# Optimization experiments

Hardware: AMD Instinct MI355X
Metric: run time of the kernel (lower is better)

Reference implementation:

```python
import jax, jax.numpy as jnp
import numpy as np
from jax import lax

D_MODEL = 1024
D_STATE = 128
D_CONV = 4
EXPAND = 2
HEADDIM = 64
D_INNER = EXPAND * D_MODEL          # 2048
NHEADS = D_INNER // HEADDIM          # 32
CONV_DIM = D_INNER + 2 * D_STATE     # 2304
D_IN_PROJ = 2 * D_INNER + 2 * D_STATE + NHEADS  # 4384
B_SZ, L_SEQ = 4, 2048
EPS = 1e-5


def setup_inputs() -> dict:
    key = jax.random.key(0)
    ks = jax.random.split(key, 10)
    x = jax.random.normal(ks[0], (B_SZ, L_SEQ, D_MODEL), dtype=jnp.float32)
    in_proj_w = jax.random.normal(ks[1], (D_IN_PROJ, D_MODEL), dtype=jnp.float32) * 0.02
    conv_w = jax.random.normal(ks[2], (CONV_DIM, D_CONV), dtype=jnp.float32) * 0.2
    conv_b = jax.random.normal(ks[3], (CONV_DIM,), dtype=jnp.float32) * 0.02
    dt_bias = jax.random.normal(ks[4], (NHEADS,), dtype=jnp.float32) * 0.5
    A_log = jnp.log(jax.random.uniform(ks[5], (NHEADS,), minval=1.0, maxval=16.0, dtype=jnp.float32))
    D = 1.0 + 0.1 * jax.random.normal(ks[6], (NHEADS,), dtype=jnp.float32)
    norm_w = jnp.ones((D_INNER,), dtype=jnp.float32)
    out_proj_w = jax.random.normal(ks[7], (D_MODEL, D_INNER), dtype=jnp.float32) * 0.02
    ln_w = jnp.ones((D_MODEL,), dtype=jnp.float32)
    ln_b = jnp.zeros((D_MODEL,), dtype=jnp.float32)
    return {"x": x, "in_proj_w": in_proj_w, "conv_w": conv_w, "conv_b": conv_b,
            "dt_bias": dt_bias, "A_log": A_log, "D": D, "norm_w": norm_w,
            "out_proj_w": out_proj_w, "ln_w": ln_w, "ln_b": ln_b}


def _mamba_block(x, in_proj_w, conv_w, conv_b, dt_bias, A_log, D, norm_w, out_proj_w, ln_w, ln_b):
    b, l, _ = x.shape
    # 1. input projection -> z, xBC, dt
    zxbcdt = jnp.einsum('bld,ed->ble', x, in_proj_w)  # (b,l,D_IN_PROJ)
    z = zxbcdt[..., :D_INNER]
    xBC = zxbcdt[..., D_INNER:D_INNER + CONV_DIM]
    dt = jax.nn.softplus(zxbcdt[..., D_INNER + CONV_DIM:] + dt_bias)  # (b,l,H)
    # 2. causal depthwise conv1d + silu
    xBC_t = xBC.transpose(0, 2, 1)  # (b,CONV_DIM,l)
    conv = lax.conv_general_dilated(xBC_t, conv_w[:, None, :], (1,), [(D_CONV - 1, 0)],
                                    feature_group_count=CONV_DIM,
                                    dimension_numbers=('NCW', 'OIW', 'NCW'))
    xBC = jax.nn.silu(conv + conv_b[:, None]).transpose(0, 2, 1)  # (b,l,CONV_DIM)
    x_ssm = xBC[..., :D_INNER].reshape(b, l, NHEADS, HEADDIM)     # (b,l,h,p)
    Bm = xBC[..., D_INNER:D_INNER + D_STATE]                      # (b,l,n) ngroups=1
    Cm = xBC[..., D_INNER + D_STATE:]                             # (b,l,n)
    # 3. selective scan
    A = -jnp.exp(A_log)               # (h,)
    dA = jnp.exp(dt * A)              # (b,l,h)
    def step(h, inp):
        dA_t, x_t, B_t, C_t, dt_t = inp  # (b,h),(b,h,p),(b,n),(b,n),(b,h)
        dBx = dt_t[:, :, None, None] * x_t[..., None] * B_t[:, None, None, :]
        h = h * dA_t[:, :, None, None] + dBx                       # (b,h,p,n)
        y = jnp.einsum('bhpn,bn->bhp', h, C_t)
        return h, y
    h0 = jnp.zeros((b, NHEADS, HEADDIM, D_STATE), dtype=x.dtype)
    inputs = (dA.transpose(1, 0, 2), x_ssm.transpose(1, 0, 2, 3),
              Bm.transpose(1, 0, 2), Cm.transpose(1, 0, 2), dt.transpose(1, 0, 2))
    _, ys = lax.scan(step, h0, inputs)                             # (l,b,h,p)
    y = ys.transpose(1, 0, 2, 3) + D[None, None, :, None] * x_ssm  # skip D term
    y = y.reshape(b, l, D_INNER)
    # 4. gated RMSNorm (norm_before_gate=False): gate first, then normalize
    y = y * jax.nn.silu(z)
    y = y * lax.rsqrt(jnp.mean(y * y, axis=-1, keepdims=True) + EPS) * norm_w
    # 5. output projection + residual
    y = jnp.einsum('bld,ed->ble', y, out_proj_w) + x
    # 6. LayerNorm (dropout is identity in eval)
    mu = jnp.mean(y, axis=-1, keepdims=True)
    var = jnp.mean((y - mu) ** 2, axis=-1, keepdims=True)
    return (y - mu) * lax.rsqrt(var + EPS) * ln_w + ln_b


def reference(x, in_proj_w, conv_w, conv_b, dt_bias, A_log, D, norm_w, out_proj_w, ln_w, ln_b):
    return _mamba_block(x, in_proj_w, conv_w, conv_b, dt_bias, A_log, D, norm_w, out_proj_w, ln_w, ln_b)
```

## Files before the change

kernel.cpp:

```cpp
#include <hip/hip_runtime.h>

typedef unsigned short u16;
typedef unsigned int   u32;

#define L_SEQ    2048
#define D_MODEL  1024
#define D_STATE  128
#define D_INNER  2048
#define NHEADS   32
#define HEADDIM  64
#define CONV_DIM 2304
#define D_IN_PROJ 4384
#define EPSF     1e-5f
#define QC       128
#define NCH      16

using frag  = __attribute__((ext_vector_type(8))) short;
using f32x4 = __attribute__((ext_vector_type(4))) float;
typedef __attribute__((ext_vector_type(8))) unsigned short u16x8;

__device__ __forceinline__ u16 f2bf(float f) {
  u32 u = __float_as_uint(f);
  return (u16)((u + 0x7fffu + ((u >> 16) & 1u)) >> 16);
}
__device__ __forceinline__ float bf2f(u16 u) {
  return __uint_as_float(((u32)u) << 16);
}
__device__ __forceinline__ void async16(const void* g, void* l) {
  __builtin_amdgcn_global_load_lds((const __attribute__((address_space(1))) u32*)g,
                                   (__attribute__((address_space(3))) u32*)l, 16, 0, 0);
}

__global__ __launch_bounds__(256) void k_cvt_all(const float* __restrict__ x,
                                                 u16* __restrict__ xb,
                                                 const float* __restrict__ w1,
                                                 u16* __restrict__ w1b,
                                                 const float* __restrict__ w2,
                                                 u16* __restrict__ w2b) {
  int bid = blockIdx.x;
  int t = threadIdx.x;
  const float* src;
  u16* dst;
  int i;
  if (bid < 8192)       { i = bid * 256 + t;          src = x;  dst = xb;  }
  else if (bid < 12576) { i = (bid - 8192) * 256 + t; src = w1; dst = w1b; }
  else if (bid < 14624) { i = (bid - 12576) * 256 + t; src = w2; dst = w2b; }
  else {
    i = (bid - 14624) * 256 + t;
    ((ushort4*)(w1b + (size_t)4384 * 1024))[i] = ushort4{0, 0, 0, 0};
    return;
  }
  float4 v = ((const float4*)src)[i];
  ushort4 o;
  o.x = f2bf(v.x); o.y = f2bf(v.y); o.z = f2bf(v.z); o.w = f2bf(v.w);
  ((ushort4*)dst)[i] = o;
}

template <int MODE>
__global__ __launch_bounds__(256) void k_gemm(const u16* __restrict__ A,
                                              const u16* __restrict__ B, int K,
                                              int Nvalid, int ldc,
                                              u16* __restrict__ Cb,
                                              float* __restrict__ Cf,
                                              const float* __restrict__ resid,
                                              float* __restrict__ Cdt) {
  __shared__ __attribute__((aligned(16))) u16 As[2][128 * 32];
  __shared__ __attribute__((aligned(16))) u16 Bs[2][128 * 32];
  const int tid = threadIdx.x;
  const int lane = tid & 63;
  const int wid = tid >> 6;
  const int wm = wid >> 1, wn = wid & 1;
  const int m0 = blockIdx.x * 128, n0 = blockIdx.y * 128;

  f32x4 acc[4][4];
#pragma unroll
  for (int i = 0; i < 4; ++i)
#pragma unroll
    for (int j = 0; j < 4; ++j) acc[i][j] = f32x4{0.f, 0.f, 0.f, 0.f};

  const char* gA[2]; const char* gB[2];
  int cbo[2];
#pragma unroll
  for (int j = 0; j < 2; ++j) {
    int base = (wid * 2 + j) * 1024;
    int p = base + lane * 16;
    int row = p >> 6;
    int colb = p & 63;
    gA[j] = (const char*)A + ((size_t)(m0 + row) * K) * 2 + colb;
    gB[j] = (const char*)B + ((size_t)(n0 + row) * K) * 2 + colb;
    cbo[j] = base;
  }

#define STAGE(bufi, kt) do { size_t kb = (size_t)(kt) * 64; \
    async16(gA[0] + kb, (char*)As[bufi] + cbo[0]); \
    async16(gA[1] + kb, (char*)As[bufi] + cbo[1]); \
    async16(gB[0] + kb, (char*)Bs[bufi] + cbo[0]); \
    async16(gB[1] + kb, (char*)Bs[bufi] + cbo[1]); } while (0)

  const int kg = (lane >> 4) * 16;
  const int rr = wm * 64 + (lane & 15);
  const int cc = wn * 64 + (lane & 15);

  STAGE(0, 0);
  const int nt = K >> 5;
  for (int t = 0; t < nt; ++t) {
    const int cur = t & 1;
    if (t + 1 < nt) {
      STAGE(cur ^ 1, t + 1);
      asm volatile("s_waitcnt vmcnt(4)" ::: "memory");
    } else {
      asm volatile("s_waitcnt vmcnt(0)" ::: "memory");
    }
    asm volatile("s_barrier" ::: "memory");
    frag af[4], bfr[4];
#pragma unroll
    for (int mi = 0; mi < 4; ++mi)
      af[mi] = *(const frag*)((const char*)As[cur] + (rr + mi * 16) * 64 + kg);
#pragma unroll
    for (int ni = 0; ni < 4; ++ni)
      bfr[ni] = *(const frag*)((const char*)Bs[cur] + (cc + ni * 16) * 64 + kg);
#pragma unroll
    for (int mi = 0; mi < 4; ++mi)
#pragma unroll
      for (int ni = 0; ni < 4; ++ni)
        acc[mi][ni] = __builtin_amdgcn_mfma_f32_16x16x32_bf16(af[mi], bfr[ni],
                                                              acc[mi][ni], 0, 0, 0);
    asm volatile("s_waitcnt lgkmcnt(0)" ::: "memory");
    asm volatile("s_barrier" ::: "memory");
  }
#undef STAGE

  const int er = (lane >> 4) * 4;
  const int ec = lane & 15;
#pragma unroll
  for (int mi = 0; mi < 4; ++mi) {
#pragma unroll
    for (int ni = 0; ni < 4; ++ni) {
      int col = n0 + wn * 64 + ni * 16 + ec;
      if (col < Nvalid) {
#pragma unroll
        for (int r = 0; r < 4; ++r) {
          int row = m0 + wm * 64 + mi * 16 + er + r;
          size_t off = (size_t)row * ldc + col;
          float v = acc[mi][ni][r];
          if (MODE == 1) {
            Cb[off] = f2bf(v);
            if (col >= D_INNER + CONV_DIM)
              Cdt[(size_t)row * NHEADS + (col - D_INNER - CONV_DIM)] = v;
          } else {
            Cf[off] = v + resid[off];
          }
        }
      }
    }
  }
}

__global__ __launch_bounds__(256) void k_convcum(const u16* __restrict__ zxb,
                                                 const float* __restrict__ cw,
                                                 const float* __restrict__ cb,
                                                 u16* __restrict__ xcb,
                                                 u16* __restrict__ bcb,
                                                 const float* __restrict__ dtf,
                                                 const float* __restrict__ dtb,
                                                 const float* __restrict__ alog,
                                                 float* __restrict__ dtv,
                                                 float* __restrict__ cumv) {
  int bid = blockIdx.x;
  if (bid < 8192) {
    int row = bid;
    int l = row & (L_SEQ - 1);
    for (int c4 = threadIdx.x; c4 < CONV_DIM / 4; c4 += 256) {
      int c = c4 * 4;
      float4 w0 = ((const float4*)cw)[c + 0];
      float4 w1 = ((const float4*)cw)[c + 1];
      float4 w2 = ((const float4*)cw)[c + 2];
      float4 w3 = ((const float4*)cw)[c + 3];
      float4 bias = *(const float4*)(cb + c);
      float a0 = bias.x, a1 = bias.y, a2 = bias.z, a3 = bias.w;
#pragma unroll
      for (int k = 0; k < 4; ++k) {
        int lm = l - 3 + k;
        if (lm >= 0) {
          ushort4 xv = *(const ushort4*)(zxb + (size_t)(row - 3 + k) * D_IN_PROJ + D_INNER + c);
          a0 = fmaf(bf2f(xv.x), (&w0.x)[k], a0);
          a1 = fmaf(bf2f(xv.y), (&w1.x)[k], a1);
          a2 = fmaf(bf2f(xv.z), (&w2.x)[k], a2);
          a3 = fmaf(bf2f(xv.w), (&w3.x)[k], a3);
        }
      }
      a0 = a0 / (1.f + __expf(-a0));
      a1 = a1 / (1.f + __expf(-a1));
      a2 = a2 / (1.f + __expf(-a2));
      a3 = a3 / (1.f + __expf(-a3));
      ushort4 o;
      o.x = f2bf(a0); o.y = f2bf(a1); o.z = f2bf(a2); o.w = f2bf(a3);
      if (c < D_INNER) {
        *(ushort4*)(xcb + (size_t)row * D_INNER + c) = o;
      } else {
        *(ushort4*)(bcb + (size_t)row * 256 + (c - D_INNER)) = o;
      }
    }
    return;
  }
  int cb_ = bid - 8192;
  int c = cb_ & (NCH - 1);
  int bh = cb_ >> 4;
  int h = bh & 31, b = bh >> 5;
  int t = threadIdx.x;
  float x = 0.f, dt = 0.f;
  if (t < 128) {
    int l = c * QC + t;
    float raw = dtf[((size_t)(b * L_SEQ + l)) * NHEADS + h] + dtb[h];
    dt = raw > 20.f ? raw : log1pf(expf(raw));
    float A = -expf(alog[h]);
    x = dt * A;
    int lane = t & 63;
#pragma unroll
    for (int off = 1; off < 64; off <<= 1) {
      float up = __shfl_up(x, off);
      if (lane >= off) x += up;
    }
  }
  __shared__ float wtot;
  if (t == 63) wtot = x;
  __syncthreads();
  if (t < 128) {
    if (t >= 64) x += wtot;
    size_t o = (size_t)bh * L_SEQ + c * QC + t;
    dtv[o] = dt;
    cumv[o] = x;
  }
}

__global__ __launch_bounds__(256) void k_g(const u16* __restrict__ bcb,
                                           u16* __restrict__ Gb) {
  __shared__ u16 Cs[128 * 128];
  __shared__ u16 Bs[128 * 128];
  int bid = blockIdx.x;
  int c = bid & (NCH - 1);
  int b = bid >> 4;
  int tid = threadIdx.x, lane = tid & 63, wid = tid >> 6;
  int wm = wid >> 1, wn = wid & 1;
  const u16* base = bcb + (size_t)(b * L_SEQ + c * QC) * 256;
  for (int idx = tid; idx < 128 * 32; idx += 256) {
    int row = idx >> 5, seg = idx & 31;
    u16x8 v = *(const u16x8*)(base + (size_t)row * 256 + seg * 8);
    if (seg < 16) *(u16x8*)&Bs[row * 128 + seg * 8] = v;
    else          *(u16x8*)&Cs[row * 128 + (seg - 16) * 8] = v;
  }
  __syncthreads();
  f32x4 acc[4][4];
#pragma unroll
  for (int i = 0; i < 4; ++i)
#pragma unroll
    for (int j = 0; j < 4; ++j) acc[i][j] = f32x4{0.f, 0.f, 0.f, 0.f};
  int rr = wm * 64 + (lane & 15);
  int cc = wn * 64 + (lane & 15);
#pragma unroll
  for (int kk = 0; kk < 4; ++kk) {
    int ko = kk * 32 + (lane >> 4) * 8;
    frag af[4], bfr[4];
#pragma unroll
    for (int mi = 0; mi < 4; ++mi)
      af[mi] = *(const frag*)&Cs[(rr + mi * 16) * 128 + ko];
#pragma unroll
    for (int ni = 0; ni < 4; ++ni)
      bfr[ni] = *(const frag*)&Bs[(cc + ni * 16) * 128 + ko];
#pragma unroll
    for (int mi = 0; mi < 4; ++mi)
#pragma unroll
      for (int ni = 0; ni < 4; ++ni)
        acc[mi][ni] = __builtin_amdgcn_mfma_f32_16x16x32_bf16(af[mi], bfr[ni],
                                                              acc[mi][ni], 0, 0, 0);
  }
  u16* gbase = Gb + ((size_t)(b * NCH + c)) * 128 * 128;
  const int er = (lane >> 4) * 4;
  const int ec = lane & 15;
#pragma unroll
  for (int mi = 0; mi < 4; ++mi)
#pragma unroll
    for (int ni = 0; ni < 4; ++ni)
#pragma unroll
      for (int r = 0; r < 4; ++r) {
        int i = wm * 64 + mi * 16 + er + r;
        int j = wn * 64 + ni * 16 + ec;
        gbase[(size_t)i * 128 + j] = f2bf(acc[mi][ni][r]);
      }
}

__global__ __launch_bounds__(256) void k_states(const u16* __restrict__ xcb,
                                                const u16* __restrict__ bcb,
                                                const float* __restrict__ dtv,
                                                const float* __restrict__ cumv,
                                                u16* __restrict__ SH) {
  __shared__ u16 XT[64 * 136];
  __shared__ u16 BW[128 * 136];
  __shared__ float wlds[128];
  int bid = blockIdx.x;
  int c = bid & (NCH - 1);
  int bh = bid >> 4;
  int h = bh & 31, b = bh >> 5;
  int tid = threadIdx.x, lane = tid & 63, wid = tid >> 6;
  int wm = wid >> 1, wn = wid & 1;
  int l0 = c * QC;
  size_t bhl = (size_t)bh * L_SEQ + l0;
  if (tid < 128) {
    float ce = cumv[bhl + 127];
    wlds[tid] = __expf(ce - cumv[bhl + tid]) * dtv[bhl + tid];
  }
  const int jrow = tid & 127;
  const u16* xbase = xcb + ((size_t)(b * L_SEQ + l0)) * D_INNER + h * HEADDIM;
  {
    int sb = (tid >> 7) * 4;
#pragma unroll
    for (int s = 0; s < 4; ++s) {
      int seg = sb + s;
      u16x8 xv = *(const u16x8*)(xbase + (size_t)jrow * D_INNER + seg * 8);
#pragma unroll
      for (int k = 0; k < 8; ++k) XT[(seg * 8 + k) * 136 + jrow] = xv[k];
    }
  }
  __syncthreads();
  const u16* bbase = bcb + (size_t)(b * L_SEQ + l0) * 256;
  {
    int sb = (tid >> 7) * 8;
    float w = wlds[jrow];
#pragma unroll
    for (int s = 0; s < 8; ++s) {
      int seg = sb + s;
      u16x8 bv = *(const u16x8*)(bbase + (size_t)jrow * 256 + seg * 8);
#pragma unroll
      for (int k = 0; k < 8; ++k)
        BW[(seg * 8 + k) * 136 + jrow] = f2bf(bf2f(bv[k]) * w);
    }
  }
  __syncthreads();
  f32x4 acc[2][4];
#pragma unroll
  for (int i = 0; i < 2; ++i)
#pragma unroll
    for (int j = 0; j < 4; ++j) acc[i][j] = f32x4{0.f, 0.f, 0.f, 0.f};
  int rr = wm * 32 + (lane & 15);
  int cc = wn * 64 + (lane & 15);
#pragma unroll
  for (int kk = 0; kk < 4; ++kk) {
    int ko = kk * 32 + (lane >> 4) * 8;
    frag af[2], bfr[4];
#pragma unroll
    for (int mi = 0; mi < 2; ++mi)
      af[mi] = *(const frag*)&XT[(rr + mi * 16) * 136 + ko];
#pragma unroll
    for (int ni = 0; ni < 4; ++ni)
      bfr[ni] = *(const frag*)&BW[(cc + ni * 16) * 136 + ko];
#pragma unroll
    for (int mi = 0; mi < 2; ++mi)
#pragma unroll
      for (int ni = 0; ni < 4; ++ni)
        acc[mi][ni] = __builtin_amdgcn_mfma_f32_16x16x32_bf16(af[mi], bfr[ni],
                                                              acc[mi][ni], 0, 0, 0);
  }
  u16* sbase = SH + ((size_t)(bh * NCH + c)) * (64 * 128);
  const int er = (lane >> 4) * 4;
  const int ec = lane & 15;
#pragma unroll
  for (int mi = 0; mi < 2; ++mi)
#pragma unroll
    for (int ni = 0; ni < 4; ++ni)
#pragma unroll
      for (int r = 0; r < 4; ++r) {
        int p = wm * 32 + mi * 16 + er + r;
        int n = wn * 64 + ni * 16 + ec;
        sbase[(size_t)p * 128 + n] = f2bf(acc[mi][ni][r]);
      }
}

__global__ __launch_bounds__(512) void k_chain(u16* __restrict__ SH,
                                               const float* __restrict__ cumv) {
  int bid = blockIdx.x;
  int half = bid & 1;
  int bh = bid >> 1;
  int t = threadIdx.x;
  u16* base = SH + (size_t)bh * NCH * 8192 + half * 4096 + t * 8;
  float H[8];
#pragma unroll
  for (int i = 0; i < 8; ++i) H[i] = 0.f;
  u16x8 s = *(const u16x8*)base;
  float e = __expf(cumv[(size_t)bh * L_SEQ + 127]);
  for (int c = 0; c < NCH; ++c) {
    u16x8 cs = s;
    float ce = e;
    if (c + 1 < NCH) {
      s = *(const u16x8*)(base + (size_t)(c + 1) * 8192);
      e = __expf(cumv[(size_t)bh * L_SEQ + (c + 1) * QC + 127]);
    }
    u16x8 h0;
#pragma unroll
    for (int k = 0; k < 8; ++k) h0[k] = f2bf(H[k]);
    *(u16x8*)(base + (size_t)c * 8192) = h0;
#pragma unroll
    for (int k = 0; k < 8; ++k) H[k] = fmaf(H[k], ce, bf2f(cs[k]));
  }
}

__global__ __launch_bounds__(256) void k_y(const u16* __restrict__ xcb,
                                           const u16* __restrict__ bcb,
                                           const float* __restrict__ dtv,
                                           const float* __restrict__ cumv,
                                           const u16* __restrict__ Gb,
                                           const u16* __restrict__ SH,
                                           u16* __restrict__ ysb) {
  __shared__ u16 Abuf[128 * 136];
  __shared__ u16 Bbuf[64 * 136];
  __shared__ float cums[128], dts[128];
  int bid = blockIdx.x;
  int c = bid & (NCH - 1);
  int bh = bid >> 4;
  int h = bh & 31, b = bh >> 5;
  int tid = threadIdx.x, lane = tid & 63, wid = tid >> 6;
  int wm = wid >> 1, wn = wid & 1;
  int l0 = c * QC;
  size_t bhl = (size_t)bh * L_SEQ + l0;
  if (tid < 128) { cums[tid] = cumv[bhl + tid]; dts[tid] = dtv[bhl + tid]; }
  const u16* xbase = xcb + ((size_t)(b * L_SEQ + l0)) * D_INNER + h * HEADDIM;
  {
    int jrow = tid & 127;
    int sb = (tid >> 7) * 4;
#pragma unroll
    for (int s = 0; s < 4; ++s) {
      int seg = sb + s;
      u16x8 xv = *(const u16x8*)(xbase + (size_t)jrow * D_INNER + seg * 8);
#pragma unroll
      for (int k = 0; k < 8; ++k) Bbuf[(seg * 8 + k) * 136 + jrow] = xv[k];
    }
  }
  __syncthreads();
  const u16* gbase = Gb + ((size_t)(b * NCH + c)) * 128 * 128;
  for (int idx = tid; idx < 128 * 16; idx += 256) {
    int i = idx >> 4, seg = idx & 15;
    u16x8 g = *(const u16x8*)(gbase + (size_t)i * 128 + seg * 8);
    float ci = cums[i];
    u16x8 o;
#pragma unroll
    for (int k = 0; k < 8; ++k) {
      int j = seg * 8 + k;
      float m = (j <= i) ? bf2f(g[k]) * __expf(ci - cums[j]) * dts[j] : 0.f;
      o[k] = f2bf(m);
    }
    *(u16x8*)&Abuf[i * 136 + seg * 8] = o;
  }
  __syncthreads();
  f32x4 acc1[4][2], acc2[4][2];
#pragma unroll
  for (int i = 0; i < 4; ++i)
#pragma unroll
    for (int j = 0; j < 2; ++j) {
      acc1[i][j] = f32x4{0.f, 0.f, 0.f, 0.f};
      acc2[i][j] = f32x4{0.f, 0.f, 0.f, 0.f};
    }
  int rr = wm * 64 + (lane & 15);
  int cc = wn * 32 + (lane & 15);
#pragma unroll
  for (int kk = 0; kk < 4; ++kk) {
    int ko = kk * 32 + (lane >> 4) * 8;
    frag af[4], bfr[2];
#pragma unroll
    for (int mi = 0; mi < 4; ++mi)
      af[mi] = *(const frag*)&Abuf[(rr + mi * 16) * 136 + ko];
#pragma unroll
    for (int ni = 0; ni < 2; ++ni)
      bfr[ni] = *(const frag*)&Bbuf[(cc + ni * 16) * 136 + ko];
#pragma unroll
    for (int mi = 0; mi < 4; ++mi)
#pragma unroll
      for (int ni = 0; ni < 2; ++ni)
        acc1[mi][ni] = __builtin_amdgcn_mfma_f32_16x16x32_bf16(af[mi], bfr[ni],
                                                               acc1[mi][ni], 0, 0, 0);
  }
  __syncthreads();
  const u16* cbase = bcb + (size_t)(b * L_SEQ + l0) * 256 + 128;
  for (int idx = tid; idx < 128 * 16; idx += 256) {
    int i = idx >> 4, seg = idx & 15;
    *(u16x8*)&Abuf[i * 136 + seg * 8] = *(const u16x8*)(cbase + (size_t)i * 256 + seg * 8);
  }
  const u16* hbase = SH + ((size_t)(bh * NCH + c)) * (64 * 128);
  for (int idx = tid; idx < 64 * 16; idx += 256) {
    int p = idx >> 4, seg = idx & 15;
    *(u16x8*)&Bbuf[p * 136 + seg * 8] = *(const u16x8*)(hbase + (size_t)p * 128 + seg * 8);
  }
  __syncthreads();
#pragma unroll
  for (int kk = 0; kk < 4; ++kk) {
    int ko = kk * 32 + (lane >> 4) * 8;
    frag af[4], bfr[2];
#pragma unroll
    for (int mi = 0; mi < 4; ++mi)
      af[mi] = *(const frag*)&Abuf[(rr + mi * 16) * 136 + ko];
#pragma unroll
    for (int ni = 0; ni < 2; ++ni)
      bfr[ni] = *(const frag*)&Bbuf[(cc + ni * 16) * 136 + ko];
#pragma unroll
    for (int mi = 0; mi < 4; ++mi)
#pragma unroll
      for (int ni = 0; ni < 2; ++ni)
        acc2[mi][ni] = __builtin_amdgcn_mfma_f32_16x16x32_bf16(af[mi], bfr[ni],
                                                               acc2[mi][ni], 0, 0, 0);
  }
  const int er = (lane >> 4) * 4;
  const int ec = lane & 15;
#pragma unroll
  for (int mi = 0; mi < 4; ++mi)
#pragma unroll
    for (int r = 0; r < 4; ++r) {
      int i = wm * 64 + mi * 16 + er + r;
      float e = __expf(cums[i]);
#pragma unroll
      for (int ni = 0; ni < 2; ++ni) {
        int p = wn * 32 + ni * 16 + ec;
        float v = acc1[mi][ni][r] + e * acc2[mi][ni][r];
        ysb[((size_t)(b * L_SEQ + l0 + i)) * D_INNER + h * HEADDIM + p] = f2bf(v);
      }
    }
}

__global__ __launch_bounds__(256) void k_gate(const u16* __restrict__ ysb,
                                              const u16* __restrict__ xcb,
                                              const u16* __restrict__ zxb,
                                              const float* __restrict__ Dp,
                                              const float* __restrict__ nw,
                                              u16* __restrict__ yb) {
  int row = blockIdx.x;
  int t = threadIdx.x;
  int d0 = t * 8;
  float Dh = Dp[d0 >> 6];
  u16x8 ya = *(const u16x8*)(ysb + (size_t)row * D_INNER + d0);
  u16x8 xa = *(const u16x8*)(xcb + (size_t)row * D_INNER + d0);
  u16x8 za = *(const u16x8*)(zxb + (size_t)row * D_IN_PROJ + d0);
  float v[8];
  float ss = 0.f;
#pragma unroll
  for (int c = 0; c < 8; ++c) {
    float val = bf2f(ya[c]) + Dh * bf2f(xa[c]);
    float zz = bf2f(za[c]);
    val *= zz / (1.f + __expf(-zz));
    v[c] = val;
    ss += val * val;
  }
  __shared__ float red[4];
#pragma unroll
  for (int off = 32; off; off >>= 1) ss += __shfl_xor(ss, off);
  if ((t & 63) == 0) red[t >> 6] = ss;
  __syncthreads();
  float tot = red[0] + red[1] + red[2] + red[3];
  float scale = rsqrtf(tot * (1.f / D_INNER) + EPSF);
  float4 w0 = *(const float4*)(nw + d0);
  float4 w1 = *(const float4*)(nw + d0 + 4);
  u16x8 o;
  o[0] = f2bf(v[0] * scale * w0.x);
  o[1] = f2bf(v[1] * scale * w0.y);
  o[2] = f2bf(v[2] * scale * w0.z);
  o[3] = f2bf(v[3] * scale * w0.w);
  o[4] = f2bf(v[4] * scale * w1.x);
  o[5] = f2bf(v[5] * scale * w1.y);
  o[6] = f2bf(v[6] * scale * w1.z);
  o[7] = f2bf(v[7] * scale * w1.w);
  *(u16x8*)(yb + (size_t)row * D_INNER + d0) = o;
}

union F4 { float4 v; float f[4]; };
__global__ __launch_bounds__(256) void k_ln(float* __restrict__ io,
                                            const float* __restrict__ lw,
                                            const float* __restrict__ lb) {
  int row = blockIdx.x;
  int t = threadIdx.x;
  int d0 = t * 4;
  F4 v; v.v = *(const float4*)(io + (size_t)row * D_MODEL + d0);
  float s1 = v.f[0] + v.f[1] + v.f[2] + v.f[3];
  float s2 = v.f[0] * v.f[0] + v.f[1] * v.f[1] + v.f[2] * v.f[2] + v.f[3] * v.f[3];
  __shared__ float r1[4], r2[4];
#pragma unroll
  for (int off = 32; off; off >>= 1) {
    s1 += __shfl_xor(s1, off);
    s2 += __shfl_xor(s2, off);
  }
  if ((t & 63) == 0) { r1[t >> 6] = s1; r2[t >> 6] = s2; }
  __syncthreads();
  float S1 = r1[0] + r1[1] + r1[2] + r1[3];
  float S2 = r2[0] + r2[1] + r2[2] + r2[3];
  float mu = S1 * (1.f / D_MODEL);
  float var = S2 * (1.f / D_MODEL) - mu * mu;
  float inv = rsqrtf(var + EPSF);
  F4 w, bb, o;
  w.v = *(const float4*)(lw + d0);
  bb.v = *(const float4*)(lb + d0);
#pragma unroll
  for (int c = 0; c < 4; ++c) o.f[c] = (v.f[c] - mu) * inv * w.f[c] + bb.f[c];
  *(float4*)(io + (size_t)row * D_MODEL + d0) = o.v;
}

extern "C" void kernel_launch(void* const* d_in, const int* in_sizes, int n_in,
                              void* d_out, int out_size, void* d_ws, size_t ws_size,
                              hipStream_t stream) {
  const float* x    = (const float*)d_in[0];
  const float* w1   = (const float*)d_in[1];
  const float* cw   = (const float*)d_in[2];
  const float* cb   = (const float*)d_in[3];
  const float* dtb  = (const float*)d_in[4];
  const float* alog = (const float*)d_in[5];
  const float* Dp   = (const float*)d_in[6];
  const float* nw   = (const float*)d_in[7];
  const float* w2   = (const float*)d_in[8];
  const float* lw   = (const float*)d_in[9];
  const float* lb   = (const float*)d_in[10];
  float* out = (float*)d_out;
  char* ws = (char*)d_ws;

  u16*   xb   = (u16*)(ws + 0);
  u16*   w1b  = (u16*)(ws + 16777216);
  u16*   w2b  = (u16*)(ws + 25952256);
  u16*   zxb  = (u16*)(ws + 30146560);
  u16*   xcb  = (u16*)(ws + 101974016);
  float* dtf  = (float*)(ws + 135528448);
  float* dtv  = (float*)(ws + 136577024);
  float* cumv = (float*)(ws + 137625600);
  u16*   ysb  = (u16*)(ws + 138674176);
  u16*   yb   = (u16*)(ws + 172228608);
  u16*   Gb   = (u16*)(ws + 205783040);
  if (ws_size < (size_t)209977344) return;

  u16* bcb = (u16*)out;
  u16* SH  = yb;

  k_cvt_all<<<14720, 256, 0, stream>>>(x, xb, w1, w1b, w2, w2b);

  k_gemm<1><<<dim3(64, 35), 256, 0, stream>>>(xb, w1b, 1024, 4384, 4384,
                                              zxb, nullptr, nullptr, dtf);

  k_convcum<<<10240, 256, 0, stream>>>(zxb, cw, cb, xcb, bcb, dtf, dtb, alog, dtv, cumv);

  k_g<<<4 * NCH, 256, 0, stream>>>(bcb, Gb);
  k_states<<<128 * NCH, 256, 0, stream>>>(xcb, bcb, dtv, cumv, SH);
  k_chain<<<256, 512, 0, stream>>>(SH, cumv);
  k_y<<<128 * NCH, 256, 0, stream>>>(xcb, bcb, dtv, cumv, Gb, SH, ysb);

  k_gate<<<8192, 256, 0, stream>>>(ysb, xcb, zxb, Dp, nw, yb);

  k_gemm<0><<<dim3(64, 8), 256, 0, stream>>>(yb, w2b, 2048, 1024, 1024,
                                             nullptr, out, x, nullptr);

  k_ln<<<8192, 256, 0, stream>>>(out, lw, lb);
}
```

Before: 348.9 us.

## Merge G and chunk-state kernels into one launch; skip upper-triangle G tiles

Merges the k_g (C·Bᵀ per chunk) and k_states kernels into a single k_ssd1 launch whose blocks branch on block index. The G work is split into two half-row blocks so each uses the same 4x2 MFMA tiling as the state blocks, and its LDS rows are padded to reduce bank conflicts. This removes one kernel launch and the tail of the small 64-block G kernel. In k_y, segments lying entirely above the causal diagonal now skip the global G load and exp computation and write zeros.

```diff
diff --git a/kernel.cpp b/kernel.cpp
--- a/kernel.cpp
+++ b/kernel.cpp
@@ -233,146 +233,148 @@
   }
 }
 
-__global__ __launch_bounds__(256) void k_g(const u16* __restrict__ bcb,
-                                           u16* __restrict__ Gb) {
-  __shared__ u16 Cs[128 * 128];
-  __shared__ u16 Bs[128 * 128];
+__global__ __launch_bounds__(256) void k_ssd1(const u16* __restrict__ xcb,
+                                              const u16* __restrict__ bcb,
+                                              const float* __restrict__ dtv,
+                                              const float* __restrict__ cumv,
+                                              u16* __restrict__ SH,
+                                              u16* __restrict__ Gb) {
+  __shared__ __attribute__((aligned(16))) char smem[52736];
   int bid = blockIdx.x;
-  int c = bid & (NCH - 1);
-  int b = bid >> 4;
   int tid = threadIdx.x, lane = tid & 63, wid = tid >> 6;
   int wm = wid >> 1, wn = wid & 1;
-  const u16* base = bcb + (size_t)(b * L_SEQ + c * QC) * 256;
-  for (int idx = tid; idx < 128 * 32; idx += 256) {
-    int row = idx >> 5, seg = idx & 31;
-    u16x8 v = *(const u16x8*)(base + (size_t)row * 256 + seg * 8);
-    if (seg < 16) *(u16x8*)&Bs[row * 128 + seg * 8] = v;
-    else          *(u16x8*)&Cs[row * 128 + (seg - 16) * 8] = v;
-  }
-  __syncthreads();
-  f32x4 acc[4][4];
-#pragma unroll
-  for (int i = 0; i < 4; ++i)
-#pragma unroll
-    for (int j = 0; j < 4; ++j) acc[i][j] = f32x4{0.f, 0.f, 0.f, 0.f};
-  int rr = wm * 64 + (lane & 15);
-  int cc = wn * 64 + (lane & 15);
-#pragma unroll
-  for (int kk = 0; kk < 4; ++kk) {
-    int ko = kk * 32 + (lane >> 4) * 8;
-    frag af[4], bfr[4];
-#pragma unroll
-    for (int mi = 0; mi < 4; ++mi)
-      af[mi] = *(const frag*)&Cs[(rr + mi * 16) * 128 + ko];
-#pragma unroll
-    for (int ni = 0; ni < 4; ++ni)
-      bfr[ni] = *(const frag*)&Bs[(cc + ni * 16) * 128 + ko];
-#pragma unroll
-    for (int mi = 0; mi < 4; ++mi)
-#pragma unroll
-      for (int ni = 0; ni < 4; ++ni)
-        acc[mi][ni] = __builtin_amdgcn_mfma_f32_16x16x32_bf16(af[mi], bfr[ni],
-                                                              acc[mi][ni], 0, 0, 0);
-  }
-  u16* gbase = Gb + ((size_t)(b * NCH + c)) * 128 * 128;
   const int er = (lane >> 4) * 4;
   const int ec = lane & 15;
-#pragma unroll
-  for (int mi = 0; mi < 4; ++mi)
-#pragma unroll
-    for (int ni = 0; ni < 4; ++ni)
-#pragma unroll
-      for (int r = 0; r < 4; ++r) {
-        int i = wm * 64 + mi * 16 + er + r;
-        int j = wn * 64 + ni * 16 + ec;
-        gbase[(size_t)i * 128 + j] = f2bf(acc[mi][ni][r]);
+
+  if (bid < 2048) {
+    u16* XT = (u16*)smem;
+    u16* BW = (u16*)(smem + 17408);
+    float* wlds = (float*)(smem + 52224);
+    int c = bid & (NCH - 1);
+    int bh = bid >> 4;
+    int h = bh & 31, b = bh >> 5;
+    int l0 = c * QC;
+    size_t bhl = (size_t)bh * L_SEQ + l0;
+    if (tid < 128) {
+      float ce = cumv[bhl + 127];
+      wlds[tid] = __expf(ce - cumv[bhl + tid]) * dtv[bhl + tid];
+    }
+    const int jrow = tid & 127;
+    const u16* xbase = xcb + ((size_t)(b * L_SEQ + l0)) * D_INNER + h * HEADDIM;
+    {
+      int sb = (tid >> 7) * 4;
+#pragma unroll
+      for (int s = 0; s < 4; ++s) {
+        int seg = sb + s;
+        u16x8 xv = *(const u16x8*)(xbase + (size_t)jrow * D_INNER + seg * 8);
+#pragma unroll
+        for (int k = 0; k < 8; ++k) XT[(seg * 8 + k) * 136 + jrow] = xv[k];
       }
-}
-
-__global__ __launch_bounds__(256) void k_states(const u16* __restrict__ xcb,
-                                                const u16* __restrict__ bcb,
-                                                const float* __restrict__ dtv,
-                                                const float* __restrict__ cumv,
-                                                u16* __restrict__ SH) {
-  __shared__ u16 XT[64 * 136];
-  __shared__ u16 BW[128 * 136];
-  __shared__ float wlds[128];
-  int bid = blockIdx.x;
-  int c = bid & (NCH - 1);
-  int bh = bid >> 4;
-  int h = bh & 31, b = bh >> 5;
-  int tid = threadIdx.x, lane = tid & 63, wid = tid >> 6;
-  int wm = wid >> 1, wn = wid & 1;
-  int l0 = c * QC;
-  size_t bhl = (size_t)bh * L_SEQ + l0;
-  if (tid < 128) {
-    float ce = cumv[bhl + 127];
-    wlds[tid] = __expf(ce - cumv[bhl + tid]) * dtv[bhl + tid];
-  }
-  const int jrow = tid & 127;
-  const u16* xbase = xcb + ((size_t)(b * L_SEQ + l0)) * D_INNER + h * HEADDIM;
-  {
-    int sb = (tid >> 7) * 4;
-#pragma unroll
-    for (int s = 0; s < 4; ++s) {
-      int seg = sb + s;
-      u16x8 xv = *(const u16x8*)(xbase + (size_t)jrow * D_INNER + seg * 8);
-#pragma unroll
-      for (int k = 0; k < 8; ++k) XT[(seg * 8 + k) * 136 + jrow] = xv[k];
-    }
-  }
-  __syncthreads();
-  const u16* bbase = bcb + (size_t)(b * L_SEQ + l0) * 256;
-  {
-    int sb = (tid >> 7) * 8;
-    float w = wlds[jrow];
-#pragma unroll
-    for (int s = 0; s < 8; ++s) {
-      int seg = sb + s;
-      u16x8 bv = *(const u16x8*)(bbase + (size_t)jrow * 256 + seg * 8);
-#pragma unroll
-      for (int k = 0; k < 8; ++k)
-        BW[(seg * 8 + k) * 136 + jrow] = f2bf(bf2f(bv[k]) * w);
-    }
-  }
-  __syncthreads();
-  f32x4 acc[2][4];
-#pragma unroll
-  for (int i = 0; i < 2; ++i)
-#pragma unroll
-    for (int j = 0; j < 4; ++j) acc[i][j] = f32x4{0.f, 0.f, 0.f, 0.f};
-  int rr = wm * 32 + (lane & 15);
-  int cc = wn * 64 + (lane & 15);
-#pragma unroll
-  for (int kk = 0; kk < 4; ++kk) {
-    int ko = kk * 32 + (lane >> 4) * 8;
-    frag af[2], bfr[4];
+    }
+    __syncthreads();
+    const u16* bbase = bcb + (size_t)(b * L_SEQ + l0) * 256;
+    {
+      int sb = (tid >> 7) * 8;
+      float w = wlds[jrow];
+#pragma unroll
+      for (int s = 0; s < 8; ++s) {
+        int seg = sb + s;
+        u16x8 bv = *(const u16x8*)(bbase + (size_t)jrow * 256 + seg * 8);
+#pragma unroll
+        for (int k = 0; k < 8; ++k)
+          BW[(seg * 8 + k) * 136 + jrow] = f2bf(bf2f(bv[k]) * w);
+      }
+    }
+    __syncthreads();
+    f32x4 acc[2][4];
+#pragma unroll
+    for (int i = 0; i < 2; ++i)
+#pragma unroll
+      for (int j = 0; j < 4; ++j) acc[i][j] = f32x4{0.f, 0.f, 0.f, 0.f};
+    int rr = wm * 32 + (lane & 15);
+    int cc = wn * 64 + (lane & 15);
+#pragma unroll
+    for (int kk = 0; kk < 4; ++kk) {
+      int ko = kk * 32 + (lane >> 4) * 8;
+      frag af[2], bfr[4];
+#pragma unroll
+      for (int mi = 0; mi < 2; ++mi)
+        af[mi] = *(const frag*)&XT[(rr + mi * 16) * 136 + ko];
+#pragma unroll
+      for (int ni = 0; ni < 4; ++ni)
+        bfr[ni] = *(const frag*)&BW[(cc + ni * 16) * 136 + ko];
+#pragma unroll
+      for (int mi = 0; mi < 2; ++mi)
+#pragma unroll
+        for (int ni = 0; ni < 4; ++ni)
+          acc[mi][ni] = __builtin_amdgcn_mfma_f32_16x16x32_bf16(af[mi], bfr[ni],
+                                                                acc[mi][ni], 0, 0, 0);
+    }
+    u16* sbase = SH + ((size_t)(bh * NCH + c)) * (64 * 128);
 #pragma unroll
     for (int mi = 0; mi < 2; ++mi)
-      af[mi] = *(const frag*)&XT[(rr + mi * 16) * 136 + ko];
-#pragma unroll
-    for (int ni = 0; ni < 4; ++ni)
-      bfr[ni] = *(const frag*)&BW[(cc + ni * 16) * 136 + ko];
+#pragma unroll
+      for (int ni = 0; ni < 4; ++ni)
+#pragma unroll
+        for (int r = 0; r < 4; ++r) {
+          int p = wm * 32 + mi * 16 + er + r;
+          int n = wn * 64 + ni * 16 + ec;
+          sbase[(size_t)p * 128 + n] = f2bf(acc[mi][ni][r]);
+        }
+  } else {
+    u16* Cs = (u16*)smem;
+    u16* Bs = (u16*)(smem + 17408);
+    int gbid = bid - 2048;
+    int half = gbid & 1;
+    int c = (gbid >> 1) & (NCH - 1);
+    int b = gbid >> 5;
+    const u16* base = bcb + (size_t)(b * L_SEQ + c * QC) * 256;
+    for (int idx = tid; idx < 128 * 16; idx += 256) {
+      int j = idx >> 4, seg = idx & 15;
+      *(u16x8*)&Bs[j * 136 + seg * 8] = *(const u16x8*)(base + (size_t)j * 256 + seg * 8);
+    }
+    for (int idx = tid; idx < 64 * 16; idx += 256) {
+      int i = idx >> 4, seg = idx & 15;
+      *(u16x8*)&Cs[i * 136 + seg * 8] =
+          *(const u16x8*)(base + (size_t)(half * 64 + i) * 256 + 128 + seg * 8);
+    }
+    __syncthreads();
+    f32x4 acc[2][4];
+#pragma unroll
+    for (int i = 0; i < 2; ++i)
+#pragma unroll
+      for (int j = 0; j < 4; ++j) acc[i][j] = f32x4{0.f, 0.f, 0.f, 0.f};
+    int rr = wm * 32 + (lane & 15);
+    int cc = wn * 64 + (lane & 15);
+#pragma unroll
+    for (int kk = 0; kk < 4; ++kk) {
+      int ko = kk * 32 + (lane >> 4) * 8;
+      frag af[2], bfr[4];
+#pragma unroll
+      for (int mi = 0; mi < 2; ++mi)
+        af[mi] = *(const frag*)&Cs[(rr + mi * 16) * 136 + ko];
+#pragma unroll
+      for (int ni = 0; ni < 4; ++ni)
+        bfr[ni] = *(const frag*)&Bs[(cc + ni * 16) * 136 + ko];
+#pragma unroll
+      for (int mi = 0; mi < 2; ++mi)
+#pragma unroll
+        for (int ni = 0; ni < 4; ++ni)
+          acc[mi][ni] = __builtin_amdgcn_mfma_f32_16x16x32_bf16(af[mi], bfr[ni],
+                                                                acc[mi][ni], 0, 0, 0);
+    }
+    u16* gbase = Gb + ((size_t)(b * NCH + c)) * 128 * 128;
 #pragma unroll
     for (int mi = 0; mi < 2; ++mi)
 #pragma unroll
       for (int ni = 0; ni < 4; ++ni)
-        acc[mi][ni] = __builtin_amdgcn_mfma_f32_16x16x32_bf16(af[mi], bfr[ni],
-                                                              acc[mi][ni], 0, 0, 0);
-  }
-  u16* sbase = SH + ((size_t)(bh * NCH + c)) * (64 * 128);
-  const int er = (lane >> 4) * 4;
-  const int ec = lane & 15;
-#pragma unroll
-  for (int mi = 0; mi < 2; ++mi)
-#pragma unroll
-    for (int ni = 0; ni < 4; ++ni)
-#pragma unroll
-      for (int r = 0; r < 4; ++r) {
-        int p = wm * 32 + mi * 16 + er + r;
-        int n = wn * 64 + ni * 16 + ec;
-        sbase[(size_t)p * 128 + n] = f2bf(acc[mi][ni][r]);
-      }
+#pragma unroll
+        for (int r = 0; r < 4; ++r) {
+          int i = half * 64 + wm * 32 + mi * 16 + er + r;
+          int j = wn * 64 + ni * 16 + ec;
+          gbase[(size_t)i * 128 + j] = f2bf(acc[mi][ni][r]);
+        }
+  }
 }
 
 __global__ __launch_bounds__(512) void k_chain(u16* __restrict__ SH,
@@ -438,16 +440,22 @@
   const u16* gbase = Gb + ((size_t)(b * NCH + c)) * 128 * 128;
   for (int idx = tid; idx < 128 * 16; idx += 256) {
     int i = idx >> 4, seg = idx & 15;
-    u16x8 g = *(const u16x8*)(gbase + (size_t)i * 128 + seg * 8);
-    float ci = cums[i];
+    int j0 = seg * 8;
     u16x8 o;
-#pragma unroll
-    for (int k = 0; k < 8; ++k) {
-      int j = seg * 8 + k;
-      float m = (j <= i) ? bf2f(g[k]) * __expf(ci - cums[j]) * dts[j] : 0.f;
-      o[k] = f2bf(m);
-    }
-    *(u16x8*)&Abuf[i * 136 + seg * 8] = o;
+    if (j0 > i) {
+#pragma unroll
+      for (int k = 0; k < 8; ++k) o[k] = 0;
+    } else {
+      u16x8 g = *(const u16x8*)(gbase + (size_t)i * 128 + j0);
+      float ci = cums[i];
+#pragma unroll
+      for (int k = 0; k < 8; ++k) {
+        int j = j0 + k;
+        float m = (j <= i) ? bf2f(g[k]) * __expf(ci - cums[j]) * dts[j] : 0.f;
+        o[k] = f2bf(m);
+      }
+    }
+    *(u16x8*)&Abuf[i * 136 + j0] = o;
   }
   __syncthreads();
   f32x4 acc1[4][2], acc2[4][2];
@@ -638,8 +646,7 @@
 
   k_convcum<<<10240, 256, 0, stream>>>(zxb, cw, cb, xcb, bcb, dtf, dtb, alog, dtv, cumv);
 
-  k_g<<<4 * NCH, 256, 0, stream>>>(bcb, Gb);
-  k_states<<<128 * NCH, 256, 0, stream>>>(xcb, bcb, dtv, cumv, SH);
+  k_ssd1<<<2048 + 128, 256, 0, stream>>>(xcb, bcb, dtv, cumv, SH, Gb);
   k_chain<<<256, 512, 0, stream>>>(SH, cumv);
   k_y<<<128 * NCH, 256, 0, stream>>>(xcb, bcb, dtv, cumv, Gb, SH, ysb);
 
```

After: 338.8 us. 1.03x faster.
